# Kernel tuning notes

Measured on AMD Instinct MI355X. Metric: run time of the kernel, lower is better.

Reference implementation:

```python
import jax, jax.numpy as jnp
import numpy as np

B, S, H = 1, 2048, 4096
NH, NKV = 32, 8          # query heads, kv heads (GQA group = 4)
HD, VHD = 128, 128       # qk head_dim, v head_dim
ROPE = 64                # partial rotary dim (head_dim * 0.5)
NEG = -1e9


def setup_inputs() -> dict:
    key = jax.random.key(0)
    ks = jax.random.split(key, 6)
    hidden_states = jax.random.normal(ks[0], (B, S, H), dtype=jnp.float32)
    # real rotary embeddings, shape [1,1,S,ROPE] so they broadcast over heads
    inv_freq = 1.0 / (10000.0 ** (jnp.arange(0, ROPE, 2, dtype=jnp.float32) / ROPE))
    freqs = jnp.arange(S, dtype=jnp.float32)[:, None] * inv_freq[None, :]  # [S, ROPE/2]
    emb = jnp.concatenate([freqs, freqs], axis=-1)                          # [S, ROPE]
    cos = jnp.cos(emb)[None, None]  # [1,1,S,ROPE]
    sin = jnp.sin(emb)[None, None]
    # additive causal mask [1,1,S,S]
    causal = jnp.tril(jnp.ones((S, S), dtype=bool))
    attention_mask = jnp.where(causal, 0.0, NEG)[None, None].astype(jnp.float32)
    w_scale = 0.02
    Wq = jax.random.normal(ks[1], (H, NH * HD), dtype=jnp.float32) * w_scale
    Wk = jax.random.normal(ks[2], (H, NKV * HD), dtype=jnp.float32) * w_scale
    Wv = jax.random.normal(ks[3], (H, NKV * VHD), dtype=jnp.float32) * w_scale
    Wo = jax.random.normal(ks[4], (NH * VHD, H), dtype=jnp.float32) * w_scale
    sinks = jax.random.normal(ks[5], (NH,), dtype=jnp.float32)
    return {"hidden_states": hidden_states, "cos": cos, "sin": sin,
            "attention_mask": attention_mask, "Wq": Wq, "Wk": Wk, "Wv": Wv,
            "Wo": Wo, "sinks": sinks}


def _rotate_half(x):
    h = x.shape[-1] // 2
    return jnp.concatenate([-x[..., h:], x[..., :h]], axis=-1)


def reference(hidden_states, cos, sin, attention_mask, Wq, Wk, Wv, Wo, sinks):
    b, s, _ = hidden_states.shape
    scaling = HD ** -0.5
    # projections -> [b, heads, s, d]
    q = (hidden_states @ Wq).reshape(b, s, NH, HD).transpose(0, 2, 1, 3)
    k = (hidden_states @ Wk).reshape(b, s, NKV, HD).transpose(0, 2, 1, 3)
    v = (hidden_states @ Wv).reshape(b, s, NKV, VHD).transpose(0, 2, 1, 3)
    # partial RoPE on the first ROPE dims
    q_r, q_n = q[..., :ROPE], q[..., ROPE:]
    k_r, k_n = k[..., :ROPE], k[..., ROPE:]
    q_r = q_r * cos + _rotate_half(q_r) * sin
    k_r = k_r * cos + _rotate_half(k_r) * sin
    q = jnp.concatenate([q_r, q_n], axis=-1)
    k = jnp.concatenate([k_r, k_n], axis=-1)
    # GQA: repeat kv heads (repeat_interleave along head dim)
    n_rep = NH // NKV
    k = jnp.repeat(k, n_rep, axis=1)  # [b, NH, s, HD]
    v = jnp.repeat(v, n_rep, axis=1)  # [b, NH, s, VHD]
    scores = jnp.einsum('bhqd,bhkd->bhqk', q, k) * scaling + attention_mask
    # attention sinks: extra logit column per head, dropped after softmax
    sink_col = jnp.broadcast_to(sinks.reshape(1, NH, 1, 1), (b, NH, s, 1))
    logits = jnp.concatenate([scores, sink_col], axis=-1)
    w = jax.nn.softmax(logits.astype(jnp.float32), axis=-1).astype(q.dtype)[..., :-1]
    attn = jnp.einsum('bhqk,bhkd->bhqd', w, v)          # [b, NH, s, VHD]
    attn = attn.transpose(0, 2, 1, 3).reshape(b, s, NH * VHD)
    return attn @ Wo
```

## Files before the change

kernel.cpp:

```cpp
#include <hip/hip_runtime.h>
#include <hip/hip_bf16.h>
#include <cstdint>
#include <cstddef>

#define S_LEN 2048
#define NHEADS 32
#define NKVH   8
#define HDIM   128

using bf16x8 = __attribute__((ext_vector_type(8))) short;
using f32x4  = __attribute__((ext_vector_type(4))) float;
using f32x16 = __attribute__((ext_vector_type(16))) float;

__device__ __forceinline__ short f2bf(float f) {
  union { float f; unsigned u; } a; a.f = f;
  unsigned u = a.u;
  unsigned r = u + 0x7fffu + ((u >> 16) & 1u);
  return (short)(r >> 16);
}
__device__ __forceinline__ unsigned pack_bf2(float lo, float hi) {
  union { float f; unsigned u; } a, b; a.f = lo; b.f = hi;
  return __builtin_amdgcn_perm(b.u, a.u, 0x07060302);
}

__device__ __forceinline__ void gld16(const void* g, void* l) {
  __builtin_amdgcn_global_load_lds((__attribute__((address_space(1))) void*)(void*)g,
                                   (__attribute__((address_space(3))) void*)l, 16, 0, 0);
}

__global__ void cvt_f32_bf16(const float* __restrict__ x, short* __restrict__ y, int n4) {
  int i = blockIdx.x * blockDim.x + threadIdx.x;
  if (i >= n4) return;
  float4 v = reinterpret_cast<const float4*>(x)[i];
  short4 o;
  o.x = f2bf(v.x); o.y = f2bf(v.y); o.z = f2bf(v.z); o.w = f2bf(v.w);
  reinterpret_cast<short4*>(y)[i] = o;
}

__global__ void transpose_to_bf16(const float* __restrict__ W, short* __restrict__ Wt,
                                  int K, int N) {
  __shared__ float tile[32][33];
  int bn = blockIdx.x * 32;
  int bk = blockIdx.y * 32;
  int tx = threadIdx.x & 31;
  int ty = (threadIdx.x >> 5) * 4;
#pragma unroll
  for (int i = 0; i < 4; ++i)
    tile[ty + i][tx] = W[(size_t)(bk + ty + i) * N + bn + tx];
  __syncthreads();
#pragma unroll
  for (int i = 0; i < 4; ++i)
    Wt[(size_t)(bn + ty + i) * K + bk + tx] = f2bf(tile[tx][ty + i]);
}

__global__ __launch_bounds__(256)
void gemm_qkv(const short* __restrict__ A, const short* __restrict__ B,
              short* __restrict__ Qb, short* __restrict__ Kb, short* __restrict__ Vtb,
              const float* __restrict__ cosb, const float* __restrict__ sinb) {
  const int K = 4096;
  __shared__ short smem[16896];
  const int bn = blockIdx.x * 128;
  const int bm = blockIdx.y * 128;
  const int t = threadIdx.x;
  const int lane = t & 63;
  const int wave = t >> 6;
  const int wm = (wave >> 1) * 64;
  const int wn = (wave & 1) * 64;
  const int lr = lane & 15;
  const int lk = (lane >> 4) * 8;

  f32x4 acc[4][4] = {};

  const int arow = t >> 2;
  const int acol = (t & 3) * 8;
  const size_t ab0 = (size_t)(bm + arow) * K + acol;
  const size_t ab1 = (size_t)(bm + 64 + arow) * K + acol;
  const size_t bb0 = (size_t)(bn + arow) * K + acol;
  const size_t bb1 = (size_t)(bn + 64 + arow) * K + acol;

  auto stage = [&](int k0, int b) {
    char* base = (char*)smem + b * 16384 + t * 16;
    gld16(A + ab0 + k0, base);
    gld16(A + ab1 + k0, base + 4096);
    gld16(B + bb0 + k0, base + 8192);
    gld16(B + bb1 + k0, base + 12288);
  };

  stage(0, 0);
  for (int it = 0; it < 128; ++it) {
    __syncthreads();
    if (it + 1 < 128) stage((it + 1) * 32, (it + 1) & 1);
    const short* Asb = smem + (it & 1) * 8192;
    const short* Bsb = Asb + 4096;
    bf16x8 af[4], bfr[4];
#pragma unroll
    for (int i = 0; i < 4; ++i)
      af[i] = *(const bf16x8*)&Asb[(wm + i * 16 + lr) * 32 + lk];
#pragma unroll
    for (int j = 0; j < 4; ++j)
      bfr[j] = *(const bf16x8*)&Bsb[(wn + j * 16 + lr) * 32 + lk];
#pragma unroll
    for (int i = 0; i < 4; ++i)
#pragma unroll
      for (int j = 0; j < 4; ++j)
        acc[i][j] = __builtin_amdgcn_mfma_f32_16x16x32_bf16(af[i], bfr[j], acc[i][j], 0, 0, 0);
  }

  const int cr = (lane >> 4) << 2;
  const int cc = lane & 15;
  const int region = (bn >= 5120) ? 2 : (bn >= 4096 ? 1 : 0);

  if (region < 2) {
    if (wn == 0) {
#pragma unroll
      for (int i = 0; i < 4; ++i) {
#pragma unroll
        for (int r = 0; r < 4; ++r) {
          int srow = bm + wm + i * 16 + cr + r;
#pragma unroll
          for (int j = 0; j < 2; ++j) {
            int c = j * 16 + cc;
            float cv = cosb[srow * 64 + c];
            float sv = sinb[srow * 64 + c];
            float x1 = acc[i][j][r], x2 = acc[i][j + 2][r];
            acc[i][j][r]     = x1 * cv - x2 * sv;
            acc[i][j + 2][r] = x2 * cv + x1 * sv;
          }
        }
      }
    }
#pragma unroll
    for (int i = 0; i < 4; ++i)
#pragma unroll
      for (int j = 0; j < 4; ++j) {
        int row = bm + wm + i * 16 + cr;
        int col = bn + wn + j * 16 + cc;
#pragma unroll
        for (int r = 0; r < 4; ++r) {
          short v = f2bf(acc[i][j][r]);
          if (region == 0) Qb[(size_t)(row + r) * 4096 + col] = v;
          else             Kb[(size_t)(row + r) * 1024 + (col - 4096)] = v;
        }
      }
  } else {
    __syncthreads();
#pragma unroll
    for (int i = 0; i < 4; ++i)
#pragma unroll
      for (int j = 0; j < 4; ++j) {
        int lc = wn + j * 16 + cc;
        int lrow = wm + i * 16 + cr;
#pragma unroll
        for (int r = 0; r < 4; ++r)
          smem[lc * 132 + lrow + r] = f2bf(acc[i][j][r]);
      }
    __syncthreads();
    const int rowl = t >> 1;
    const int off = (t & 1) * 64;
    short* dst = Vtb + (size_t)(bn - 5120 + rowl) * 2048 + bm + off;
#pragma unroll
    for (int c = 0; c < 8; ++c)
      *(bf16x8*)(dst + c * 8) = *(const bf16x8*)&smem[rowl * 132 + off + c * 8];
  }
}

__global__ __launch_bounds__(256)
void gemm_out(const short* __restrict__ A, const short* __restrict__ B,
              float* __restrict__ C) {
  const int K = 4096, N = 4096;
  __shared__ short smem[16384];
  const int bn = blockIdx.x * 128;
  const int bm = blockIdx.y * 128;
  const int t = threadIdx.x;
  const int lane = t & 63;
  const int wave = t >> 6;
  const int wm = (wave >> 1) * 64;
  const int wn = (wave & 1) * 64;
  const int lr = lane & 15;
  const int lk = (lane >> 4) * 8;

  f32x4 acc[4][4] = {};

  const int arow = t >> 2;
  const int acol = (t & 3) * 8;
  const size_t ab0 = (size_t)(bm + arow) * K + acol;
  const size_t ab1 = (size_t)(bm + 64 + arow) * K + acol;
  const size_t bb0 = (size_t)(bn + arow) * K + acol;
  const size_t bb1 = (size_t)(bn + 64 + arow) * K + acol;

  auto stage = [&](int k0, int b) {
    char* base = (char*)smem + b * 16384 + t * 16;
    gld16(A + ab0 + k0, base);
    gld16(A + ab1 + k0, base + 4096);
    gld16(B + bb0 + k0, base + 8192);
    gld16(B + bb1 + k0, base + 12288);
  };

  stage(0, 0);
  for (int it = 0; it < 128; ++it) {
    __syncthreads();
    if (it + 1 < 128) stage((it + 1) * 32, (it + 1) & 1);
    const short* Asb = smem + (it & 1) * 8192;
    const short* Bsb = Asb + 4096;
    bf16x8 af[4], bfr[4];
#pragma unroll
    for (int i = 0; i < 4; ++i)
      af[i] = *(const bf16x8*)&Asb[(wm + i * 16 + lr) * 32 + lk];
#pragma unroll
    for (int j = 0; j < 4; ++j)
      bfr[j] = *(const bf16x8*)&Bsb[(wn + j * 16 + lr) * 32 + lk];
#pragma unroll
    for (int i = 0; i < 4; ++i)
#pragma unroll
      for (int j = 0; j < 4; ++j)
        acc[i][j] = __builtin_amdgcn_mfma_f32_16x16x32_bf16(af[i], bfr[j], acc[i][j], 0, 0, 0);
  }

  const int cr = (lane >> 4) << 2;
  const int cc = lane & 15;
#pragma unroll
  for (int i = 0; i < 4; ++i)
#pragma unroll
    for (int j = 0; j < 4; ++j) {
      int row = bm + wm + i * 16 + cr;
      int col = bn + wn + j * 16 + cc;
#pragma unroll
      for (int r = 0; r < 4; ++r)
        C[(size_t)(row + r) * N + col] = acc[i][j][r];
    }
}

__global__ __launch_bounds__(256, 2)
void attn_kernel(const short* __restrict__ Q, const short* __restrict__ Kg,
                 const short* __restrict__ Vg, const float* __restrict__ sinks,
                 short* __restrict__ O) {
  __shared__ short lds[32768];
  const int h = blockIdx.x;
  const int qt = 15 - blockIdx.y;
  const int q0 = qt * 128;
  const int kvh = h >> 2;
  const int t = threadIdx.x;
  const int lane = t & 63;
  const int w = t >> 6;
  const int l31 = lane & 31;
  const int l7 = lane & 7;
  const bool qh = lane >= 32;
  const int q5 = qh ? 1 : 0;
  const int nkt = 2 * qt + 2;

  const int kch = (t & 15) ^ ((t >> 4) & 7);
  const short* kgb = Kg + (size_t)(t >> 4) * 1024 + kvh * 128 + kch * 8;
  const int vch = (t & 7) ^ ((t >> 3) & 7);
  const short* vgb = Vg + (size_t)(kvh * 128 + (t >> 3)) * 2048 + vch * 8;

  auto stage = [&](int kt, int b) {
    short* kl = lds + b * 16384 + t * 8;
    short* vl = lds + b * 16384 + 8192 + t * 8;
    const short* kg = kgb + (size_t)kt * 64 * 1024;
    const short* vg = vgb + kt * 64;
#pragma unroll
    for (int c = 0; c < 4; ++c) {
      gld16(kg + (size_t)c * 16 * 1024, kl + c * 2048);
      gld16(vg + (size_t)c * 32 * 2048, vl + c * 2048);
    }
  };

  const short* qp = Q + (size_t)(q0 + w * 32 + l31) * 4096 + h * 128 + q5 * 8;
  bf16x8 qf[8];
#pragma unroll
  for (int st = 0; st < 8; ++st) qf[st] = *(const bf16x8*)(qp + st * 16);

  union { short s[8]; bf16x8 v; } ones;
#pragma unroll
  for (int i = 0; i < 8; ++i) ones.s[i] = (short)0x3F80;

  f32x16 acc[4] = {};
  f32x16 lacc = {};

  stage(0, 0);
  const int qg = q0 + w * 32 + l31;
  const float ce = 0.12751743f;

  for (int kt = 0; kt < nkt; ++kt) {
    const int b = kt & 1;
    __syncthreads();
    if (kt + 1 < nkt) stage(kt + 1, b ^ 1);
    const short* Ks = lds + b * 16384;
    const short* Vs = Ks + 8192;

    f32x16 sa0 = {}, sa1 = {};
#pragma unroll
    for (int st = 0; st < 8; ++st) {
      const int cp = ((st * 2 + q5) ^ l7) * 8;
      bf16x8 k0 = *(const bf16x8*)(Ks + (l31) * 128 + cp);
      bf16x8 k1 = *(const bf16x8*)(Ks + (32 + l31) * 128 + cp);
      sa0 = __builtin_amdgcn_mfma_f32_32x32x16_bf16(k0, qf[st], sa0, 0, 0, 0);
      sa1 = __builtin_amdgcn_mfma_f32_32x32x16_bf16(k1, qf[st], sa1, 0, 0, 0);
    }

    if (kt >= 2 * qt) {
      const int kb0 = kt * 64 + q5 * 4;
#pragma unroll
      for (int r = 0; r < 16; ++r) {
        int kg0 = kb0 + ((r >> 2) << 3) + (r & 3);
        float s0 = (kg0 <= qg) ? sa0[r] * ce : -INFINITY;
        float s1 = (kg0 + 32 <= qg) ? sa1[r] * ce : -INFINITY;
        sa0[r] = __builtin_amdgcn_exp2f(s0);
        sa1[r] = __builtin_amdgcn_exp2f(s1);
      }
    } else {
#pragma unroll
      for (int r = 0; r < 16; ++r) {
        sa0[r] = __builtin_amdgcn_exp2f(sa0[r] * ce);
        sa1[r] = __builtin_amdgcn_exp2f(sa1[r] * ce);
      }
    }

#pragma unroll
    for (int s = 0; s < 4; ++s) {
      const f32x16& S = (s & 2) ? sa1 : sa0;
      float a0, a1, a2, a3, b0, b1, b2, b3;
      if (s & 1) {
        a0 = qh ? S[12] : S[8];  a1 = qh ? S[13] : S[9];
        a2 = qh ? S[14] : S[10]; a3 = qh ? S[15] : S[11];
        b0 = qh ? S[8]  : S[12]; b1 = qh ? S[9]  : S[13];
        b2 = qh ? S[10] : S[14]; b3 = qh ? S[11] : S[15];
      } else {
        a0 = qh ? S[4] : S[0]; a1 = qh ? S[5] : S[1];
        a2 = qh ? S[6] : S[2]; a3 = qh ? S[7] : S[3];
        b0 = qh ? S[0] : S[4]; b1 = qh ? S[1] : S[5];
        b2 = qh ? S[2] : S[6]; b3 = qh ? S[3] : S[7];
      }
      unsigned d0 = pack_bf2(a0, a1), d1 = pack_bf2(a2, a3);
      unsigned e0 = pack_bf2(b0, b1), e1 = pack_bf2(b2, b3);
      unsigned r0 = (unsigned)__shfl_xor((int)e0, 32, 64);
      unsigned r1 = (unsigned)__shfl_xor((int)e1, 32, 64);
      union { unsigned u[4]; bf16x8 v; } P;
      P.u[0] = qh ? r0 : d0;  P.u[1] = qh ? r1 : d1;
      P.u[2] = qh ? d0 : r0;  P.u[3] = qh ? d1 : r1;

      lacc = __builtin_amdgcn_mfma_f32_32x32x16_bf16(ones.v, P.v, lacc, 0, 0, 0);
#pragma unroll
      for (int m = 0; m < 4; ++m) {
        bf16x8 vf = *(const bf16x8*)(Vs + (m * 32 + l31) * 64 + (((s * 2 + q5) ^ l7) * 8));
        acc[m] = __builtin_amdgcn_mfma_f32_32x32x16_bf16(vf, P.v, acc[m], 0, 0, 0);
      }
    }
  }

  float denom = lacc[0] + __builtin_amdgcn_exp2f(sinks[h] * 1.4426950f);
  float rinv = 1.0f / denom;

  __syncthreads();
#pragma unroll
  for (int m = 0; m < 4; ++m) {
#pragma unroll
    for (int r = 0; r < 16; ++r) {
      int d = m * 32 + ((r >> 2) << 3) + q5 * 4 + (r & 3);
      int ql = w * 32 + l31;
      lds[ql * 128 + (((d >> 3) ^ l7) << 3) + (d & 7)] = f2bf(acc[m][r] * rinv);
    }
  }
  __syncthreads();
  const int qrow = t >> 1;
  const int half = (t & 1) * 8;
  short* ob = O + (size_t)(q0 + qrow) * 4096 + h * 128;
#pragma unroll
  for (int cc = 0; cc < 8; ++cc) {
    int chunk = half + cc;
    bf16x8 v = *(const bf16x8*)&lds[qrow * 128 + ((chunk ^ (qrow & 7)) << 3)];
    *(bf16x8*)(ob + chunk * 8) = v;
  }
}

extern "C" void kernel_launch(void* const* d_in, const int* in_sizes, int n_in,
                              void* d_out, int out_size, void* d_ws, size_t ws_size,
                              hipStream_t stream) {
  const float* hs    = (const float*)d_in[0];
  const float* cosb  = (const float*)d_in[1];
  const float* sinb  = (const float*)d_in[2];
  const float* Wq    = (const float*)d_in[4];
  const float* Wk    = (const float*)d_in[5];
  const float* Wv    = (const float*)d_in[6];
  const float* Wo    = (const float*)d_in[7];
  const float* sinks = (const float*)d_in[8];
  float* out = (float*)d_out;

  char* ws = (char*)d_ws;
  short* Xb    = (short*)ws;
  short* Wqkvt = (short*)(ws + 16777216);
  short* Qb    = (short*)(ws + 67108864);
  short* Kb    = (short*)(ws + 83886080);
  short* Vtb   = (short*)(ws + 88080384);
  short* Ab    = Xb;
  short* Wot   = Wqkvt;

  cvt_f32_bf16<<<8192, 256, 0, stream>>>(hs, Xb, 2097152);
  transpose_to_bf16<<<dim3(128, 128), 256, 0, stream>>>(Wq, Wqkvt, 4096, 4096);
  transpose_to_bf16<<<dim3(32, 128), 256, 0, stream>>>(Wk, Wqkvt + (size_t)4096 * 4096, 4096, 1024);
  transpose_to_bf16<<<dim3(32, 128), 256, 0, stream>>>(Wv, Wqkvt + (size_t)5120 * 4096, 4096, 1024);

  gemm_qkv<<<dim3(48, 16), 256, 0, stream>>>(Xb, Wqkvt, Qb, Kb, Vtb, cosb, sinb);

  transpose_to_bf16<<<dim3(128, 128), 256, 0, stream>>>(Wo, Wot, 4096, 4096);

  attn_kernel<<<dim3(32, 16), 256, 0, stream>>>(Qb, Kb, Vtb, sinks, Ab);

  gemm_out<<<dim3(32, 16), 256, 0, stream>>>(Ab, Wot, out);
}
```

Measured before the change: 510.6 us.

## Double K-tile depth in output GEMM with XOR-swizzled LDS and vectorize transpose

Measured after the change: 490.6 us. 3.9% less time.

```diff
diff --git a/kernel.cpp b/kernel.cpp
--- a/kernel.cpp
+++ b/kernel.cpp
@@ -37,20 +37,26 @@
   reinterpret_cast<short4*>(y)[i] = o;
 }
 
-__global__ void transpose_to_bf16(const float* __restrict__ W, short* __restrict__ Wt,
-                                  int K, int N) {
-  __shared__ float tile[32][33];
-  int bn = blockIdx.x * 32;
-  int bk = blockIdx.y * 32;
-  int tx = threadIdx.x & 31;
-  int ty = (threadIdx.x >> 5) * 4;
-#pragma unroll
-  for (int i = 0; i < 4; ++i)
-    tile[ty + i][tx] = W[(size_t)(bk + ty + i) * N + bn + tx];
+__global__ __launch_bounds__(256)
+void transpose_to_bf16(const float* __restrict__ W, short* __restrict__ Wt,
+                       int K, int N) {
+  __shared__ float tile[32 * 33];
+  const int bn = blockIdx.x * 32, bk = blockIdx.y * 32;
+  const int t = threadIdx.x;
+  const int c4 = t & 7, kr = t >> 3;
+  float4 v = *(const float4*)&W[(size_t)(bk + kr) * N + bn + c4 * 4];
+  tile[kr * 33 + c4 * 4 + 0] = v.x;
+  tile[kr * 33 + c4 * 4 + 1] = v.y;
+  tile[kr * 33 + c4 * 4 + 2] = v.z;
+  tile[kr * 33 + c4 * 4 + 3] = v.w;
   __syncthreads();
-#pragma unroll
-  for (int i = 0; i < 4; ++i)
-    Wt[(size_t)(bn + ty + i) * K + bk + tx] = f2bf(tile[tx][ty + i]);
+  const int k4 = t & 7, nr = t >> 3;
+  short4 o;
+  o.x = f2bf(tile[(k4 * 4 + 0) * 33 + nr]);
+  o.y = f2bf(tile[(k4 * 4 + 1) * 33 + nr]);
+  o.z = f2bf(tile[(k4 * 4 + 2) * 33 + nr]);
+  o.w = f2bf(tile[(k4 * 4 + 3) * 33 + nr]);
+  *(short4*)&Wt[(size_t)(bn + nr) * K + bk + k4 * 4] = o;
 }
 
 __global__ __launch_bounds__(256)
@@ -164,11 +170,11 @@
   }
 }
 
-__global__ __launch_bounds__(256)
+__global__ __launch_bounds__(256, 2)
 void gemm_out(const short* __restrict__ A, const short* __restrict__ B,
               float* __restrict__ C) {
   const int K = 4096, N = 4096;
-  __shared__ short smem[16384];
+  __shared__ short smem[32768];
   const int bn = blockIdx.x * 128;
   const int bm = blockIdx.y * 128;
   const int t = threadIdx.x;
@@ -177,43 +183,49 @@
   const int wm = (wave >> 1) * 64;
   const int wn = (wave & 1) * 64;
   const int lr = lane & 15;
-  const int lk = (lane >> 4) * 8;
+  const int lk3 = lane >> 4;
 
   f32x4 acc[4][4] = {};
 
-  const int arow = t >> 2;
-  const int acol = (t & 3) * 8;
-  const size_t ab0 = (size_t)(bm + arow) * K + acol;
-  const size_t ab1 = (size_t)(bm + 64 + arow) * K + acol;
-  const size_t bb0 = (size_t)(bn + arow) * K + acol;
-  const size_t bb1 = (size_t)(bn + 64 + arow) * K + acol;
+  const int srow = t >> 3;
+  const int sch = (t & 7) ^ ((srow & 1) << 2);
+  const size_t ab = (size_t)(bm + srow) * K + sch * 8;
+  const size_t bb = (size_t)(bn + srow) * K + sch * 8;
 
   auto stage = [&](int k0, int b) {
-    char* base = (char*)smem + b * 16384 + t * 16;
-    gld16(A + ab0 + k0, base);
-    gld16(A + ab1 + k0, base + 4096);
-    gld16(B + bb0 + k0, base + 8192);
-    gld16(B + bb1 + k0, base + 12288);
+    short* dst = smem + b * 16384 + t * 8;
+#pragma unroll
+    for (int p = 0; p < 4; ++p) {
+      gld16(A + ab + k0 + (size_t)(p * 32) * K, dst + p * 2048);
+      gld16(B + bb + k0 + (size_t)(p * 32) * K, dst + 8192 + p * 2048);
+    }
   };
 
   stage(0, 0);
-  for (int it = 0; it < 128; ++it) {
+  for (int it = 0; it < 64; ++it) {
     __syncthreads();
-    if (it + 1 < 128) stage((it + 1) * 32, (it + 1) & 1);
-    const short* Asb = smem + (it & 1) * 8192;
-    const short* Bsb = Asb + 4096;
-    bf16x8 af[4], bfr[4];
-#pragma unroll
-    for (int i = 0; i < 4; ++i)
-      af[i] = *(const bf16x8*)&Asb[(wm + i * 16 + lr) * 32 + lk];
-#pragma unroll
-    for (int j = 0; j < 4; ++j)
-      bfr[j] = *(const bf16x8*)&Bsb[(wn + j * 16 + lr) * 32 + lk];
-#pragma unroll
-    for (int i = 0; i < 4; ++i)
-#pragma unroll
-      for (int j = 0; j < 4; ++j)
-        acc[i][j] = __builtin_amdgcn_mfma_f32_16x16x32_bf16(af[i], bfr[j], acc[i][j], 0, 0, 0);
+    if (it + 1 < 64) stage((it + 1) * 64, (it + 1) & 1);
+    const short* Asb = smem + (it & 1) * 16384;
+    const short* Bsb = Asb + 8192;
+#pragma unroll
+    for (int h = 0; h < 2; ++h) {
+      bf16x8 af[4], bfr[4];
+#pragma unroll
+      for (int i = 0; i < 4; ++i) {
+        int row = wm + i * 16 + lr;
+        af[i] = *(const bf16x8*)&Asb[row * 64 + (((h * 4 + lk3) ^ ((row & 1) << 2)) * 8)];
+      }
+#pragma unroll
+      for (int j = 0; j < 4; ++j) {
+        int row = wn + j * 16 + lr;
+        bfr[j] = *(const bf16x8*)&Bsb[row * 64 + (((h * 4 + lk3) ^ ((row & 1) << 2)) * 8)];
+      }
+#pragma unroll
+      for (int i = 0; i < 4; ++i)
+#pragma unroll
+        for (int j = 0; j < 4; ++j)
+          acc[i][j] = __builtin_amdgcn_mfma_f32_16x16x32_bf16(af[i], bfr[j], acc[i][j], 0, 0, 0);
+    }
   }
 
   const int cr = (lane >> 4) << 2;
```
